# Performance work log

Hardware: AMD Instinct MI355X
Metric: run time of the kernel (lower is better)

Reference implementation:

```python
import jax, jax.numpy as jnp
import numpy as np

INPUT, HIDDEN = 8, 16

def setup_inputs() -> dict:
    key = jax.random.key(0)
    ks = jax.random.split(key, 7)
    s_ih = 1.0 / np.sqrt(HIDDEN)
    x = jax.random.normal(ks[0], (8192, 512, INPUT), dtype=jnp.float32)
    W_ih = jax.random.uniform(ks[1], (HIDDEN, INPUT), jnp.float32, -s_ih, s_ih)
    W_hh = jax.random.uniform(ks[2], (HIDDEN, HIDDEN), jnp.float32, -s_ih, s_ih)
    b_ih = jax.random.uniform(ks[3], (HIDDEN,), jnp.float32, -s_ih, s_ih)
    b_hh = jax.random.uniform(ks[4], (HIDDEN,), jnp.float32, -s_ih, s_ih)
    s_fc = 1.0 / np.sqrt(HIDDEN)
    fc_w = jax.random.uniform(ks[5], (1, HIDDEN), jnp.float32, -s_fc, s_fc)
    fc_b = jax.random.uniform(ks[6], (1,), jnp.float32, -s_fc, s_fc)
    return {"x": x, "W_ih": W_ih, "W_hh": W_hh, "b_ih": b_ih, "b_hh": b_hh, "fc_w": fc_w, "fc_b": fc_b}

def reference(x, W_ih, W_hh, b_ih, b_hh, fc_w, fc_b):
    B, T, _ = x.shape
    # Precompute input projection for all timesteps: [B, T, H]
    xp = jnp.einsum('bti,hi->bth', x, W_ih) + b_ih + b_hh
    h0 = jnp.zeros((B, HIDDEN), dtype=x.dtype)

    def step(h, xt):
        h_new = jnp.tanh(xt + h @ W_hh.T)
        return h_new, None

    h_last, _ = jax.lax.scan(step, h0, jnp.swapaxes(xp, 0, 1))
    return h_last @ fc_w.T + fc_b  # [B, 1]
```

## Files before the change

### kernel.cpp

```cpp
#include <hip/hip_runtime.h>


#define RNN_B   8192
#define RNN_T   512
#define RNN_IN  8
#define RNN_H   16
#define TC      32
#define NB      16
#define XSTRIDE 264
#define HP      20

__global__ __launch_bounds__(256, 2) void rnn_fused_kernel(
    const float* __restrict__ x,
    const float* __restrict__ W_ih,
    const float* __restrict__ W_hh,
    const float* __restrict__ b_ih,
    const float* __restrict__ b_hh,
    const float* __restrict__ fc_w,
    const float* __restrict__ fc_b,
    float* __restrict__ out)
{
    __shared__ float xs[NB * XSTRIDE];
    __shared__ float hbuf[NB * HP];

    const int tid = (int)threadIdx.x;
    const int j   = tid & 15;
    const int g   = tid >> 4;
    const int b0  = (int)blockIdx.x * NB;
    const int b   = b0 + g;

    float whh[RNN_H];
#pragma unroll
    for (int k = 0; k < RNN_H; k += 4) {
        float4 w = *(const float4*)(W_hh + j * RNN_H + k);
        whh[k] = w.x; whh[k+1] = w.y; whh[k+2] = w.z; whh[k+3] = w.w;
    }
    float wih[RNN_IN];
#pragma unroll
    for (int i = 0; i < RNN_IN; i += 4) {
        float4 w = *(const float4*)(W_ih + j * RNN_IN + i);
        wih[i] = w.x; wih[i+1] = w.y; wih[i+2] = w.z; wih[i+3] = w.w;
    }
    const float bias = b_ih[j] + b_hh[j];

    hbuf[g * HP + j] = 0.0f;

    float hlast = 0.0f;

    for (int t0 = 0; t0 < RNN_T; t0 += TC) {
        __syncthreads();
#pragma unroll
        for (int p = 0; p < 4; ++p) {
            int idx = tid + p * 256;
            int row = idx >> 6;
            int off = idx & 63;
            float4 v = *(const float4*)(x + ((size_t)(b0 + row) * RNN_T + t0) * RNN_IN + off * 4);
            *(float4*)(xs + row * XSTRIDE + off * 4) = v;
        }
        __syncthreads();

#pragma unroll 4
        for (int tt = 0; tt < TC; ++tt) {
            const float* xp = xs + g * XSTRIDE + tt * RNN_IN;
            const float4 xa = *(const float4*)(xp);
            const float4 xb = *(const float4*)(xp + 4);
            const float4 h0 = *(const float4*)(hbuf + g * HP + 0);
            const float4 h1 = *(const float4*)(hbuf + g * HP + 4);
            const float4 h2 = *(const float4*)(hbuf + g * HP + 8);
            const float4 h3 = *(const float4*)(hbuf + g * HP + 12);

            float a0 = fmaf(wih[0], xa.x, bias);
            a0 = fmaf(wih[1], xa.y, a0);
            a0 = fmaf(wih[2], xa.z, a0);
            a0 = fmaf(wih[3], xa.w, a0);
            a0 = fmaf(whh[0], h0.x, a0);
            a0 = fmaf(whh[1], h0.y, a0);

            float a1 = wih[4] * xb.x;
            a1 = fmaf(wih[5], xb.y, a1);
            a1 = fmaf(wih[6], xb.z, a1);
            a1 = fmaf(wih[7], xb.w, a1);
            a1 = fmaf(whh[2], h0.z, a1);
            a1 = fmaf(whh[3], h0.w, a1);

            float a2 = whh[4] * h1.x;
            a2 = fmaf(whh[5],  h1.y, a2);
            a2 = fmaf(whh[6],  h1.z, a2);
            a2 = fmaf(whh[7],  h1.w, a2);
            a2 = fmaf(whh[8],  h2.x, a2);
            a2 = fmaf(whh[9],  h2.y, a2);

            float a3 = whh[10] * h2.z;
            a3 = fmaf(whh[11], h2.w, a3);
            a3 = fmaf(whh[12], h3.x, a3);
            a3 = fmaf(whh[13], h3.y, a3);
            a3 = fmaf(whh[14], h3.z, a3);
            a3 = fmaf(whh[15], h3.w, a3);

            const float s = (a0 + a1) + (a2 + a3);

            const float e  = __expf(s + s);
            const float r  = __builtin_amdgcn_rcpf(e + 1.0f);
            const float hn = fmaf(-2.0f, r, 1.0f);

            hbuf[g * HP + j] = hn;
            hlast = hn;
        }
    }

    float v = hlast * fc_w[j];
    v += __shfl_xor(v, 1);
    v += __shfl_xor(v, 2);
    v += __shfl_xor(v, 4);
    v += __shfl_xor(v, 8);
    if (j == 0) out[b] = v + fc_b[0];
}

extern "C" void kernel_launch(void* const* d_in, const int* in_sizes, int n_in,
                              void* d_out, int out_size, void* d_ws, size_t ws_size,
                              hipStream_t stream)
{
    const float* x    = (const float*)d_in[0];
    const float* W_ih = (const float*)d_in[1];
    const float* W_hh = (const float*)d_in[2];
    const float* b_ih = (const float*)d_in[3];
    const float* b_hh = (const float*)d_in[4];
    const float* fc_w = (const float*)d_in[5];
    const float* fc_b = (const float*)d_in[6];
    float* out = (float*)d_out;

    dim3 grid(RNN_B / NB);
    dim3 block(256);
    rnn_fused_kernel<<<grid, block, 0, stream>>>(x, W_ih, W_hh, b_ih, b_hh, fc_w, fc_b, out);
}
```

Baseline: 239.2 us.

## Double-buffer x tiles via global_load_lds and exchange hidden state with DPP rotates

Stages input tiles directly into LDS with async global_load_lds into a double buffer, prefetching the next tile while the current one is computed, so each tile costs one barrier instead of two. The hidden state is no longer passed through LDS; it is broadcast within each 16-lane row using DPP row-rotate gathers, with W_hh columns permuted to match. tanh now uses exp2 with a folded constant. The aim is to take LDS round-trips and barriers off the serial recurrence, at the cost of 15 DPP moves per step and reliance on async load completion semantics.

```diff
diff --git a/kernel.cpp b/kernel.cpp
--- a/kernel.cpp
+++ b/kernel.cpp
@@ -1,4 +1,5 @@
 #include <hip/hip_runtime.h>
+#include <stdint.h>
 
 
 #define RNN_B   8192
@@ -8,7 +9,52 @@
 #define TC      32
 #define NB      16
 #define XSTRIDE 264
-#define HP      20
+#define NTILE   (RNN_T / TC)
+#define BUFSZ   (NB * XSTRIDE)
+
+#if defined(__has_builtin)
+#if __has_builtin(__builtin_amdgcn_mov_dpp)
+#define ROR16(x, N) ((uint32_t)__builtin_amdgcn_mov_dpp((int)(x), 0x120 + (N), 0xF, 0xF, false))
+#endif
+#endif
+#ifndef ROR16
+#define ROR16(x, N) ((uint32_t)__builtin_amdgcn_update_dpp(0, (int)(x), 0x120 + (N), 0xF, 0xF, false))
+#endif
+
+__device__ __forceinline__ void gather16(uint32_t in, uint32_t v[16]) {
+    v[0]  = in;
+    v[8]  = ROR16(v[0], 8);
+    v[4]  = ROR16(v[0], 4);
+    v[12] = ROR16(v[8], 4);
+    v[2]  = ROR16(v[0], 2);
+    v[6]  = ROR16(v[4], 2);
+    v[10] = ROR16(v[8], 2);
+    v[14] = ROR16(v[12], 2);
+    v[1]  = ROR16(v[0], 1);
+    v[3]  = ROR16(v[2], 1);
+    v[5]  = ROR16(v[4], 1);
+    v[7]  = ROR16(v[6], 1);
+    v[9]  = ROR16(v[8], 1);
+    v[11] = ROR16(v[10], 1);
+    v[13] = ROR16(v[12], 1);
+    v[15] = ROR16(v[14], 1);
+}
+
+__device__ __forceinline__ void stage_tile(const float* __restrict__ x,
+                                           float* lds_base, int b0, int t0,
+                                           int wv, int lane)
+{
+#pragma unroll
+    for (int p = 0; p < 4; ++p) {
+        const int row = wv + 4 * p;
+        const float* gp = x + ((size_t)(b0 + row) * RNN_T + t0) * RNN_IN + lane * 4;
+        float* lp = lds_base + row * XSTRIDE;
+        __builtin_amdgcn_global_load_lds(
+            (const __attribute__((address_space(1))) uint32_t*)gp,
+            (__attribute__((address_space(3))) uint32_t*)lp,
+            16, 0, 0);
+    }
+}
 
 __global__ __launch_bounds__(256, 2) void rnn_fused_kernel(
     const float* __restrict__ x,
@@ -20,21 +66,22 @@
     const float* __restrict__ fc_b,
     float* __restrict__ out)
 {
-    __shared__ float xs[NB * XSTRIDE];
-    __shared__ float hbuf[NB * HP];
+    __shared__ float xs[2 * BUFSZ];
 
-    const int tid = (int)threadIdx.x;
-    const int j   = tid & 15;
-    const int g   = tid >> 4;
-    const int b0  = (int)blockIdx.x * NB;
-    const int b   = b0 + g;
+    const int tid  = (int)threadIdx.x;
+    const int j    = tid & 15;
+    const int g    = tid >> 4;
+    const int wv   = tid >> 6;
+    const int lane = tid & 63;
+    const int b0   = (int)blockIdx.x * NB;
+    const int b    = b0 + g;
 
+    uint32_t sv[16];
+    gather16((uint32_t)j, sv);
     float whh[RNN_H];
 #pragma unroll
-    for (int k = 0; k < RNN_H; k += 4) {
-        float4 w = *(const float4*)(W_hh + j * RNN_H + k);
-        whh[k] = w.x; whh[k+1] = w.y; whh[k+2] = w.z; whh[k+3] = w.w;
-    }
+    for (int m = 0; m < 16; ++m) whh[m] = W_hh[j * RNN_H + (int)sv[m]];
+
     float wih[RNN_IN];
 #pragma unroll
     for (int i = 0; i < RNN_IN; i += 4) {
@@ -43,77 +90,70 @@
     }
     const float bias = b_ih[j] + b_hh[j];
 
-    hbuf[g * HP + j] = 0.0f;
+    stage_tile(x, xs, b0, 0, wv, lane);
+    __syncthreads();
 
-    float hlast = 0.0f;
+    float hn = 0.0f;
 
-    for (int t0 = 0; t0 < RNN_T; t0 += TC) {
-        __syncthreads();
-#pragma unroll
-        for (int p = 0; p < 4; ++p) {
-            int idx = tid + p * 256;
-            int row = idx >> 6;
-            int off = idx & 63;
-            float4 v = *(const float4*)(x + ((size_t)(b0 + row) * RNN_T + t0) * RNN_IN + off * 4);
-            *(float4*)(xs + row * XSTRIDE + off * 4) = v;
-        }
-        __syncthreads();
+    for (int tile = 0; tile < NTILE; ++tile) {
+        const int cur = tile & 1;
+        if (tile + 1 < NTILE)
+            stage_tile(x, xs + (cur ^ 1) * BUFSZ, b0, (tile + 1) * TC, wv, lane);
 
-#pragma unroll 4
+        const float* xg = xs + cur * BUFSZ + g * XSTRIDE;
+
+#pragma unroll 8
         for (int tt = 0; tt < TC; ++tt) {
-            const float* xp = xs + g * XSTRIDE + tt * RNN_IN;
+            const float* xp = xg + tt * RNN_IN;
             const float4 xa = *(const float4*)(xp);
             const float4 xb = *(const float4*)(xp + 4);
-            const float4 h0 = *(const float4*)(hbuf + g * HP + 0);
-            const float4 h1 = *(const float4*)(hbuf + g * HP + 4);
-            const float4 h2 = *(const float4*)(hbuf + g * HP + 8);
-            const float4 h3 = *(const float4*)(hbuf + g * HP + 12);
+
+            uint32_t v[16];
+            gather16(__float_as_uint(hn), v);
 
             float a0 = fmaf(wih[0], xa.x, bias);
             a0 = fmaf(wih[1], xa.y, a0);
             a0 = fmaf(wih[2], xa.z, a0);
             a0 = fmaf(wih[3], xa.w, a0);
-            a0 = fmaf(whh[0], h0.x, a0);
-            a0 = fmaf(whh[1], h0.y, a0);
+            a0 = fmaf(whh[0], __uint_as_float(v[0]), a0);
+            a0 = fmaf(whh[1], __uint_as_float(v[1]), a0);
+            a0 = fmaf(whh[2], __uint_as_float(v[2]), a0);
+            a0 = fmaf(whh[3], __uint_as_float(v[3]), a0);
 
             float a1 = wih[4] * xb.x;
             a1 = fmaf(wih[5], xb.y, a1);
             a1 = fmaf(wih[6], xb.z, a1);
             a1 = fmaf(wih[7], xb.w, a1);
-            a1 = fmaf(whh[2], h0.z, a1);
-            a1 = fmaf(whh[3], h0.w, a1);
+            a1 = fmaf(whh[4], __uint_as_float(v[4]), a1);
+            a1 = fmaf(whh[5], __uint_as_float(v[5]), a1);
+            a1 = fmaf(whh[6], __uint_as_float(v[6]), a1);
+            a1 = fmaf(whh[7], __uint_as_float(v[7]), a1);
 
-            float a2 = whh[4] * h1.x;
-            a2 = fmaf(whh[5],  h1.y, a2);
-            a2 = fmaf(whh[6],  h1.z, a2);
-            a2 = fmaf(whh[7],  h1.w, a2);
-            a2 = fmaf(whh[8],  h2.x, a2);
-            a2 = fmaf(whh[9],  h2.y, a2);
+            float a2 = whh[8] * __uint_as_float(v[8]);
+            a2 = fmaf(whh[9],  __uint_as_float(v[9]),  a2);
+            a2 = fmaf(whh[10], __uint_as_float(v[10]), a2);
+            a2 = fmaf(whh[11], __uint_as_float(v[11]), a2);
 
-            float a3 = whh[10] * h2.z;
-            a3 = fmaf(whh[11], h2.w, a3);
-            a3 = fmaf(whh[12], h3.x, a3);
-            a3 = fmaf(whh[13], h3.y, a3);
-            a3 = fmaf(whh[14], h3.z, a3);
-            a3 = fmaf(whh[15], h3.w, a3);
+            float a3 = whh[12] * __uint_as_float(v[12]);
+            a3 = fmaf(whh[13], __uint_as_float(v[13]), a3);
+            a3 = fmaf(whh[14], __uint_as_float(v[14]), a3);
+            a3 = fmaf(whh[15], __uint_as_float(v[15]), a3);
 
-            const float s = (a0 + a1) + (a2 + a3);
+            const float s = (a0 + a2) + (a1 + a3);
 
-            const float e  = __expf(s + s);
+            const float e  = __builtin_amdgcn_exp2f(s * 2.8853900817779268f);
             const float r  = __builtin_amdgcn_rcpf(e + 1.0f);
-            const float hn = fmaf(-2.0f, r, 1.0f);
-
-            hbuf[g * HP + j] = hn;
-            hlast = hn;
+            hn = fmaf(-2.0f, r, 1.0f);
         }
+        __syncthreads();
     }
 
-    float v = hlast * fc_w[j];
-    v += __shfl_xor(v, 1);
-    v += __shfl_xor(v, 2);
-    v += __shfl_xor(v, 4);
-    v += __shfl_xor(v, 8);
-    if (j == 0) out[b] = v + fc_b[0];
+    float vsum = hn * fc_w[j];
+    vsum += __shfl_xor(vsum, 1);
+    vsum += __shfl_xor(vsum, 2);
+    vsum += __shfl_xor(vsum, 4);
+    vsum += __shfl_xor(vsum, 8);
+    if (j == 0) out[b] = vsum + fc_b[0];
 }
 
 extern "C" void kernel_launch(void* const* d_in, const int* in_sizes, int n_in,
```

Result: slower. 250.3 us (+4.6%).
